# Kernel optimization log

Hardware: AMD Instinct MI355X
Metric: run time of the kernel (lower is better)

Reference implementation:

```python
import jax, jax.numpy as jnp
import numpy as np

N_USERS = 50000
N_ITEMS = 100000
N_GROUPS = 20000
D = 128
NNZ_U = 1000000
NNZ_I = 2000000
NNZ_F = 3000000


def setup_inputs() -> dict:
    key = jax.random.key(0)
    ks = jax.random.split(key, 14)
    user_emb = jax.random.normal(ks[0], (N_USERS, D), jnp.float32)
    item_emb = jax.random.normal(ks[1], (N_ITEMS, D), jnp.float32)
    group_emb = jax.random.normal(ks[2], (N_GROUPS, D), jnp.float32)
    # user hypergraph incidence [N_GROUPS, N_USERS] in COO
    u_rows = jax.random.randint(ks[3], (NNZ_U,), 0, N_GROUPS)
    u_cols = jax.random.randint(ks[4], (NNZ_U,), 0, N_USERS)
    u_vals = jax.random.uniform(ks[5], (NNZ_U,), jnp.float32)
    # item hypergraph incidence [N_GROUPS, N_ITEMS] in COO
    i_rows = jax.random.randint(ks[6], (NNZ_I,), 0, N_GROUPS)
    i_cols = jax.random.randint(ks[7], (NNZ_I,), 0, N_ITEMS)
    i_vals = jax.random.uniform(ks[8], (NNZ_I,), jnp.float32)
    # full hypergraph [N_USERS+N_ITEMS, N_GROUPS] in COO
    f_rows = jax.random.randint(ks[9], (NNZ_F,), 0, N_USERS + N_ITEMS)
    f_cols = jax.random.randint(ks[10], (NNZ_F,), 0, N_GROUPS)
    f_vals = jax.random.uniform(ks[11], (NNZ_F,), jnp.float32)
    # nn.Linear(2D, D): weight [D, 2D], bias [D]
    W_agg = jax.random.normal(ks[12], (D, 2 * D), jnp.float32) * 0.05
    b_agg = jnp.zeros((D,), jnp.float32)
    return dict(user_emb=user_emb, item_emb=item_emb, group_emb=group_emb,
                u_rows=u_rows, u_cols=u_cols, u_vals=u_vals,
                i_rows=i_rows, i_cols=i_cols, i_vals=i_vals,
                f_rows=f_rows, f_cols=f_cols, f_vals=f_vals,
                W_agg=W_agg, b_agg=b_agg)


def _spmm(rows, cols, vals, dense, num_rows):
    # sparse[rows, cols]=vals (COO) @ dense -> [num_rows, d]
    return jax.ops.segment_sum(vals[:, None] * dense[cols], rows, num_segments=num_rows)


def reference(user_emb, item_emb, group_emb,
              u_rows, u_cols, u_vals,
              i_rows, i_cols, i_vals,
              f_rows, f_cols, f_vals,
              W_agg, b_agg):
    user_msg = _spmm(u_rows, u_cols, u_vals, user_emb, N_GROUPS)   # [G, D]
    item_msg = _spmm(i_rows, i_cols, i_vals, item_emb, N_GROUPS)   # [G, D]
    msg = jnp.concatenate([user_msg, item_msg], axis=1) @ W_agg.T + b_agg  # [G, D]
    norm_emb = _spmm(f_rows, f_cols, f_vals, msg, N_USERS + N_ITEMS)       # [U+I, D]
    return (norm_emb, msg)
```

## Files before the change

kernel.cpp:

```cpp
#include <hip/hip_runtime.h>
#include <hip/hip_bf16.h>
#include <stdint.h>

#define N_USERS  50000
#define N_ITEMS  100000
#define N_GROUPS 20000
#define DIM      128
#define TWO_DIM  256
#define N_FULL   (N_USERS + N_ITEMS)

#define NBU  625
#define NBI  1250
#define NBF  2344
#define NBT  (NBU + NBI + NBF)
#define CAP  2048

#define TILE_E 32768
#define NT     184
#define NT_PER_XCD 23

__global__ __launch_bounds__(256) void spmm_atomic(
    const int* __restrict__ rows, const int* __restrict__ cols,
    const float* __restrict__ vals, const float* __restrict__ dense,
    float* __restrict__ out, int nnz)
{
    long long t = (long long)blockIdx.x * blockDim.x + threadIdx.x;
    int e    = (int)(t >> 5);
    int lane = (int)(t & 31);
    if (e >= nnz) return;
    int   r = rows[e];
    int   c = cols[e];
    float v = vals[e];
    float4 x = ((const float4*)(dense + (size_t)c * DIM))[lane];
    float* dst = out + (size_t)r * DIM + lane * 4;
    atomicAdd(dst + 0, v * x.x);
    atomicAdd(dst + 1, v * x.y);
    atomicAdd(dst + 2, v * x.z);
    atomicAdd(dst + 3, v * x.w);
}


__device__ __forceinline__ int bucket_of(long long t,
    const int* __restrict__ u_rows, int nnz_u,
    const int* __restrict__ i_rows, int nnz_i,
    const int* __restrict__ f_rows)
{
    if (t < nnz_u)                          return u_rows[t] >> 5;
    else if (t < (long long)nnz_u + nnz_i)  return NBU + (i_rows[t - nnz_u] >> 4);
    else                                    return NBU + NBI + (f_rows[t - nnz_u - nnz_i] >> 6);
}

__global__ __launch_bounds__(512) void hist_tiles(
    const int* __restrict__ u_rows, int nnz_u,
    const int* __restrict__ i_rows, int nnz_i,
    const int* __restrict__ f_rows, int nnz_f,
    unsigned short* __restrict__ M)
{
    __shared__ int h[NBT];
    int tid = threadIdx.x;
    for (int i = tid; i < NBT; i += 512) h[i] = 0;
    __syncthreads();
    int t = (blockIdx.x & 7) * NT_PER_XCD + (blockIdx.x >> 3);
    long long total = (long long)nnz_u + nnz_i + nnz_f;
    long long base  = (long long)t * TILE_E;
    for (int j = tid; j < TILE_E; j += 512) {
        long long e = base + j;
        if (e >= total) break;
        atomicAdd(&h[bucket_of(e, u_rows, nnz_u, i_rows, nnz_i, f_rows)], 1);
    }
    __syncthreads();
    unsigned short* Mrow = M + (size_t)t * NBT;
    for (int i = tid; i < NBT; i += 512) Mrow[i] = (unsigned short)h[i];
}

__global__ __launch_bounds__(64) void tile_prefix(
    unsigned short* __restrict__ M, int* __restrict__ btot)
{
    int b = blockIdx.x * 64 + threadIdx.x;
    if (b >= NBT) return;
    int run = 0;
#pragma unroll 1
    for (int t = 0; t < NT; t += 4) {
        size_t i0 = (size_t)(t + 0) * NBT + b;
        size_t i1 = (size_t)(t + 1) * NBT + b;
        size_t i2 = (size_t)(t + 2) * NBT + b;
        size_t i3 = (size_t)(t + 3) * NBT + b;
        int v0 = M[i0], v1 = M[i1], v2 = M[i2], v3 = M[i3];
        M[i0] = (unsigned short)run; run += v0;
        M[i1] = (unsigned short)run; run += v1;
        M[i2] = (unsigned short)run; run += v2;
        M[i3] = (unsigned short)run; run += v3;
    }
    btot[b] = run;
}

__global__ __launch_bounds__(256) void scan_buckets(
    const int* __restrict__ btot, int* __restrict__ bptr)
{
    __shared__ int wsum[4];
    __shared__ int s_carry;
    int tid = threadIdx.x, lane = tid & 63, wave = tid >> 6;
    if (tid == 0) s_carry = 0;
    __syncthreads();
    for (int base = 0; base < NBT; base += 256) {
        int b = base + tid;
        int x = (b < NBT) ? btot[b] : 0;
        int incl = x;
#pragma unroll
        for (int off = 1; off < 64; off <<= 1) {
            int y = __shfl_up(incl, off, 64);
            if (lane >= off) incl += y;
        }
        if (lane == 63) wsum[wave] = incl;
        __syncthreads();
        int waveOff = 0;
        for (int w = 0; w < wave; ++w) waveOff += wsum[w];
        int carry = s_carry;
        int ex = carry + waveOff + incl - x;
        if (b < NBT) bptr[b] = ex;
        __syncthreads();
        if (tid == 255) s_carry = carry + waveOff + incl;
        __syncthreads();
    }
    if (tid == 0) bptr[NBT] = s_carry;
}

__global__ __launch_bounds__(512) void scatter_tiles(
    const int* __restrict__ u_rows, const int* __restrict__ u_cols,
    const float* __restrict__ u_vals, int nnz_u,
    const int* __restrict__ i_rows, const int* __restrict__ i_cols,
    const float* __restrict__ i_vals, int nnz_i,
    const int* __restrict__ f_rows, const int* __restrict__ f_cols,
    const float* __restrict__ f_vals, int nnz_f,
    const unsigned short* __restrict__ M, const int* __restrict__ bptr,
    uint2* __restrict__ pack)
{
    __shared__ int cur[NBT];
    int tid = threadIdx.x;
    int t = (blockIdx.x & 7) * NT_PER_XCD + (blockIdx.x >> 3);
    const unsigned short* Mrow = M + (size_t)t * NBT;
    for (int i = tid; i < NBT; i += 512) cur[i] = bptr[i] + (int)Mrow[i];
    __syncthreads();
    long long total = (long long)nnz_u + nnz_i + nnz_f;
    long long base  = (long long)t * TILE_E;
    for (int j = tid; j < TILE_E; j += 512) {
        long long e = base + j;
        if (e >= total) break;
        int b, lrow, col; float v;
        if (e < nnz_u) {
            int k = (int)e; int r = u_rows[k];
            b = r >> 5; lrow = r & 31; col = u_cols[k]; v = u_vals[k];
        } else if (e < (long long)nnz_u + nnz_i) {
            int k = (int)(e - nnz_u); int r = i_rows[k];
            b = NBU + (r >> 4); lrow = r & 15; col = i_cols[k]; v = i_vals[k];
        } else {
            int k = (int)(e - nnz_u - nnz_i); int r = f_rows[k];
            b = NBU + NBI + (r >> 6); lrow = r & 63; col = f_cols[k]; v = f_vals[k];
        }
        int p = atomicAdd(&cur[b], 1);
        pack[p] = make_uint2(((unsigned)lrow << 17) | (unsigned)col, __float_as_uint(v));
    }
}

__global__ __launch_bounds__(256) void gather_buckets(
    const int* __restrict__ bptr, const uint2* __restrict__ pack,
    const float4* __restrict__ denseA, float* __restrict__ outA,
    int nbA, int rowsA, int nrowsA, int baseA,
    const float4* __restrict__ denseB, float* __restrict__ outB,
    int rowsB, int nrowsB, int baseB)
{
    __shared__ uint2 sE[CAP];
    __shared__ int   h[64];
    __shared__ int   o[65];

    const float4* dense; float* out; int rowsPB, nrows, lb, bid;
    if ((int)blockIdx.x < nbA) {
        dense = denseA; out = outA; rowsPB = rowsA; nrows = nrowsA;
        lb = blockIdx.x; bid = baseA + lb;
    } else {
        dense = denseB; out = outB; rowsPB = rowsB; nrows = nrowsB;
        lb = blockIdx.x - nbA; bid = baseB + lb;
    }
    int tid = threadIdx.x;
    if (tid < 64) h[tid] = 0;
    __syncthreads();

    int p0 = bptr[bid], p1 = bptr[bid + 1];
    int cnt = p1 - p0;

    for (int j = tid; j < cnt; j += 256)
        atomicAdd(&h[pack[p0 + j].x >> 17], 1);
    __syncthreads();

    if (tid < 64) {
        int x = (tid < rowsPB) ? h[tid] : 0;
        int incl = x;
#pragma unroll
        for (int off = 1; off < 64; off <<= 1) {
            int y = __shfl_up(incl, off, 64);
            if ((tid & 63) >= off) incl += y;
        }
        o[tid + 1] = incl;
        if (tid == 0) o[0] = 0;
        h[tid] = incl - x;
    }
    __syncthreads();

    for (int j = tid; j < cnt; j += 256) {
        uint2 e = pack[p0 + j];
        int r = e.x >> 17;
        int p = atomicAdd(&h[r], 1);
        sE[p] = make_uint2(e.x & 0x1FFFF, e.y);
    }
    __syncthreads();

    int wave = tid >> 6, lane = tid & 63, half = lane >> 5, sl = lane & 31;
    float4* out4 = (float4*)out;
    for (int r = wave; r < rowsPB; r += 4) {
        int s = o[r], epos = o[r + 1];
        float4 a0 = make_float4(0.f, 0.f, 0.f, 0.f);
        float4 a1 = a0, a2 = a0, a3 = a0;
        for (int base = s; base < epos; base += 8) {
            int j0 = base + half, j1 = base + 2 + half;
            int j2 = base + 4 + half, j3 = base + 6 + half;
            if (j0 < epos) {
                uint2 e = sE[j0]; float v = __uint_as_float(e.y);
                float4 x = dense[(size_t)e.x * 32 + sl];
                a0.x = fmaf(v, x.x, a0.x); a0.y = fmaf(v, x.y, a0.y);
                a0.z = fmaf(v, x.z, a0.z); a0.w = fmaf(v, x.w, a0.w);
            }
            if (j1 < epos) {
                uint2 e = sE[j1]; float v = __uint_as_float(e.y);
                float4 x = dense[(size_t)e.x * 32 + sl];
                a1.x = fmaf(v, x.x, a1.x); a1.y = fmaf(v, x.y, a1.y);
                a1.z = fmaf(v, x.z, a1.z); a1.w = fmaf(v, x.w, a1.w);
            }
            if (j2 < epos) {
                uint2 e = sE[j2]; float v = __uint_as_float(e.y);
                float4 x = dense[(size_t)e.x * 32 + sl];
                a2.x = fmaf(v, x.x, a2.x); a2.y = fmaf(v, x.y, a2.y);
                a2.z = fmaf(v, x.z, a2.z); a2.w = fmaf(v, x.w, a2.w);
            }
            if (j3 < epos) {
                uint2 e = sE[j3]; float v = __uint_as_float(e.y);
                float4 x = dense[(size_t)e.x * 32 + sl];
                a3.x = fmaf(v, x.x, a3.x); a3.y = fmaf(v, x.y, a3.y);
                a3.z = fmaf(v, x.z, a3.z); a3.w = fmaf(v, x.w, a3.w);
            }
        }
        float4 acc;
        acc.x = (a0.x + a1.x) + (a2.x + a3.x);
        acc.y = (a0.y + a1.y) + (a2.y + a3.y);
        acc.z = (a0.z + a1.z) + (a2.z + a3.z);
        acc.w = (a0.w + a1.w) + (a2.w + a3.w);
        acc.x += __shfl_xor(acc.x, 32, 64);
        acc.y += __shfl_xor(acc.y, 32, 64);
        acc.z += __shfl_xor(acc.z, 32, 64);
        acc.w += __shfl_xor(acc.w, 32, 64);
        int row = lb * rowsPB + r;
        if (half == 0 && row < nrows)
            out4[(size_t)row * 32 + sl] = acc;
    }
}

__global__ __launch_bounds__(256) void dense_agg(
    const float* __restrict__ um, const float* __restrict__ im,
    const float* __restrict__ W, const float* __restrict__ b,
    float* __restrict__ msg)
{
    __shared__ float As[32][68];
    __shared__ float Ws[64][132];

    int tid = threadIdx.x;
    int tx  = tid & 15;
    int ty  = tid >> 4;
    int rowBase = blockIdx.x * 32;

    float acc[2][8];
#pragma unroll
    for (int i = 0; i < 2; ++i)
#pragma unroll
        for (int j = 0; j < 8; ++j) acc[i][j] = 0.f;

    for (int kc = 0; kc < 4; ++kc) {
        int k0 = kc * 64;
        const float* Asrc = (k0 < DIM) ? um : im;
        int kOff = (k0 < DIM) ? k0 : (k0 - DIM);

#pragma unroll
        for (int l = 0; l < 2; ++l) {
            int idx = tid + l * 256;
            int r   = idx >> 4;
            int kq  = idx & 15;
            int gRow = rowBase + r;
            float4 v = make_float4(0.f, 0.f, 0.f, 0.f);
            if (gRow < N_GROUPS)
                v = *(const float4*)(Asrc + (size_t)gRow * DIM + kOff + kq * 4);
            *(float4*)&As[r][kq * 4] = v;
        }
#pragma unroll
        for (int l = 0; l < 8; ++l) {
            int idx = tid + l * 256;
            int d   = idx >> 4;
            int kq  = idx & 15;
            float4 v = *(const float4*)(W + (size_t)d * TWO_DIM + k0 + kq * 4);
            Ws[kq * 4 + 0][d] = v.x;
            Ws[kq * 4 + 1][d] = v.y;
            Ws[kq * 4 + 2][d] = v.z;
            Ws[kq * 4 + 3][d] = v.w;
        }
        __syncthreads();

        int ty2 = ty * 2;
        int tx8 = tx * 8;
#pragma unroll 8
        for (int k = 0; k < 64; ++k) {
            float a0 = As[ty2 + 0][k];
            float a1 = As[ty2 + 1][k];
            float4 w0 = *(const float4*)&Ws[k][tx8];
            float4 w1 = *(const float4*)&Ws[k][tx8 + 4];
            acc[0][0] = fmaf(a0, w0.x, acc[0][0]);
            acc[0][1] = fmaf(a0, w0.y, acc[0][1]);
            acc[0][2] = fmaf(a0, w0.z, acc[0][2]);
            acc[0][3] = fmaf(a0, w0.w, acc[0][3]);
            acc[0][4] = fmaf(a0, w1.x, acc[0][4]);
            acc[0][5] = fmaf(a0, w1.y, acc[0][5]);
            acc[0][6] = fmaf(a0, w1.z, acc[0][6]);
            acc[0][7] = fmaf(a0, w1.w, acc[0][7]);
            acc[1][0] = fmaf(a1, w0.x, acc[1][0]);
            acc[1][1] = fmaf(a1, w0.y, acc[1][1]);
            acc[1][2] = fmaf(a1, w0.z, acc[1][2]);
            acc[1][3] = fmaf(a1, w0.w, acc[1][3]);
            acc[1][4] = fmaf(a1, w1.x, acc[1][4]);
            acc[1][5] = fmaf(a1, w1.y, acc[1][5]);
            acc[1][6] = fmaf(a1, w1.z, acc[1][6]);
            acc[1][7] = fmaf(a1, w1.w, acc[1][7]);
        }
        __syncthreads();
    }

    int d0 = tx * 8;
    float4 bv0 = *(const float4*)(b + d0);
    float4 bv1 = *(const float4*)(b + d0 + 4);
#pragma unroll
    for (int i = 0; i < 2; ++i) {
        int gRow = rowBase + ty * 2 + i;
        if (gRow < N_GROUPS) {
            float4 o0 = make_float4(acc[i][0] + bv0.x, acc[i][1] + bv0.y,
                                    acc[i][2] + bv0.z, acc[i][3] + bv0.w);
            float4 o1 = make_float4(acc[i][4] + bv1.x, acc[i][5] + bv1.y,
                                    acc[i][6] + bv1.z, acc[i][7] + bv1.w);
            *(float4*)(msg + (size_t)gRow * DIM + d0)     = o0;
            *(float4*)(msg + (size_t)gRow * DIM + d0 + 4) = o1;
        }
    }
}

extern "C" void kernel_launch(void* const* d_in, const int* in_sizes, int n_in,
                              void* d_out, int out_size, void* d_ws, size_t ws_size,
                              hipStream_t stream)
{
    const float* user_emb = (const float*)d_in[0];
    const float* item_emb = (const float*)d_in[1];
    const int*   u_rows = (const int*)d_in[3];
    const int*   u_cols = (const int*)d_in[4];
    const float* u_vals = (const float*)d_in[5];
    const int*   i_rows = (const int*)d_in[6];
    const int*   i_cols = (const int*)d_in[7];
    const float* i_vals = (const float*)d_in[8];
    const int*   f_rows = (const int*)d_in[9];
    const int*   f_cols = (const int*)d_in[10];
    const float* f_vals = (const float*)d_in[11];
    const float* W      = (const float*)d_in[12];
    const float* bias   = (const float*)d_in[13];

    int nnz_u = in_sizes[3];
    int nnz_i = in_sizes[6];
    int nnz_f = in_sizes[9];
    long long nnz_tot = (long long)nnz_u + nnz_i + nnz_f;

    float* out  = (float*)d_out;
    float* norm = out;
    float* msg  = out + (size_t)N_FULL * DIM;

    float* um = norm;
    float* im = norm + (size_t)N_GROUPS * DIM;

    auto ceil16 = [](size_t b) { return (b + 15) & ~(size_t)15; };
    size_t need = 0;
    size_t o_M    = need; need += ceil16((size_t)NT * NBT * 2);
    size_t o_btot = need; need += ceil16((size_t)NBT * 4);
    size_t o_bptr = need; need += ceil16((size_t)(NBT + 1) * 4);
    size_t o_pack = need; need += ceil16((size_t)nnz_tot * 8);

    if (ws_size >= need && nnz_tot <= (long long)NT * TILE_E) {
        uint8_t* ws = (uint8_t*)d_ws;
        unsigned short* M = (unsigned short*)(ws + o_M);
        int*   btot = (int*)(ws + o_btot);
        int*   bptr = (int*)(ws + o_bptr);
        uint2* pack = (uint2*)(ws + o_pack);

        hist_tiles<<<NT, 512, 0, stream>>>(
            u_rows, nnz_u, i_rows, nnz_i, f_rows, nnz_f, M);

        tile_prefix<<<(NBT + 63) / 64, 64, 0, stream>>>(M, btot);

        scan_buckets<<<1, 256, 0, stream>>>(btot, bptr);

        scatter_tiles<<<NT, 512, 0, stream>>>(
            u_rows, u_cols, u_vals, nnz_u,
            i_rows, i_cols, i_vals, nnz_i,
            f_rows, f_cols, f_vals, nnz_f,
            M, bptr, pack);

        gather_buckets<<<NBU + NBI, 256, 0, stream>>>(
            bptr, pack,
            (const float4*)user_emb, um, NBU, 32, N_GROUPS, 0,
            (const float4*)item_emb, im, 16, N_GROUPS, NBU);

        dense_agg<<<(N_GROUPS + 31) / 32, 256, 0, stream>>>(um, im, W, bias, msg);

        gather_buckets<<<NBF, 256, 0, stream>>>(
            bptr, pack,
            (const float4*)msg, norm, NBF, 64, N_FULL, NBU + NBI,
            (const float4*)msg, norm, 64, N_FULL, NBU + NBI);
    } else {
        hipMemsetAsync(norm, 0, (size_t)N_FULL * DIM * sizeof(float), stream);
        auto spmm_blocks = [](int nnz) {
            return (unsigned)(((long long)nnz * 32 + 255) / 256);
        };
        spmm_atomic<<<spmm_blocks(nnz_u), 256, 0, stream>>>(
            u_rows, u_cols, u_vals, user_emb, um, nnz_u);
        spmm_atomic<<<spmm_blocks(nnz_i), 256, 0, stream>>>(
            i_rows, i_cols, i_vals, item_emb, im, nnz_i);
        dense_agg<<<(N_GROUPS + 31) / 32, 256, 0, stream>>>(um, im, W, bias, msg);
        hipMemsetAsync(norm, 0, (size_t)2 * N_GROUPS * DIM * sizeof(float), stream);
        spmm_atomic<<<spmm_blocks(nnz_f), 256, 0, stream>>>(
            f_rows, f_cols, f_vals, msg, norm, nnz_f);
    }
}
```

Baseline: 821.6 us.

## Gather dense rows from bf16 copies of embeddings and msg in SpMM

Converts user and item embeddings to bf16 in the workspace with a new conversion kernel, and has dense_agg also write a bf16 copy of msg. The gather SpMM kernels then read half-width rows and widen them to fp32 before the FMA, which halves the random-gather traffic. In exchange it adds two conversion passes over the 150k x 128 embedding tables on every call and needs more workspace. It also loses precision on the inputs, which may break tolerance.

```diff
diff --git a/kernel.cpp b/kernel.cpp
--- a/kernel.cpp
+++ b/kernel.cpp
@@ -18,6 +18,26 @@
 #define TILE_E 32768
 #define NT     184
 #define NT_PER_XCD 23
+
+__device__ __forceinline__ unsigned bf16_rne(float f)
+{
+    unsigned u = __float_as_uint(f);
+    return (u + 0x7FFFu + ((u >> 16) & 1u)) >> 16;
+}
+__device__ __forceinline__ unsigned bf16_pack(float a, float b)
+{
+    return bf16_rne(a) | (bf16_rne(b) << 16);
+}
+
+__global__ __launch_bounds__(256) void f32_to_bf16(
+    const float4* __restrict__ src, uint2* __restrict__ dst, int n4)
+{
+    int stride = gridDim.x * 256;
+    for (int i = blockIdx.x * 256 + threadIdx.x; i < n4; i += stride) {
+        float4 v = src[i];
+        dst[i] = make_uint2(bf16_pack(v.x, v.y), bf16_pack(v.z, v.w));
+    }
+}
 
 __global__ __launch_bounds__(256) void spmm_atomic(
     const int* __restrict__ rows, const int* __restrict__ cols,
@@ -38,7 +58,6 @@
     atomicAdd(dst + 2, v * x.z);
     atomicAdd(dst + 3, v * x.w);
 }
-
 
 __device__ __forceinline__ int bucket_of(long long t,
     const int* __restrict__ u_rows, int nnz_u,
@@ -162,18 +181,38 @@
     }
 }
 
+template<bool BF16>
+__device__ __forceinline__ void edge_fma(
+    const void* __restrict__ dense, unsigned col, int sl, float v, float4& a)
+{
+    if constexpr (BF16) {
+        uint2 q = ((const uint2*)dense)[(size_t)col * 32 + sl];
+        float x0 = __uint_as_float(q.x << 16);
+        float x1 = __uint_as_float(q.x & 0xFFFF0000u);
+        float x2 = __uint_as_float(q.y << 16);
+        float x3 = __uint_as_float(q.y & 0xFFFF0000u);
+        a.x = fmaf(v, x0, a.x); a.y = fmaf(v, x1, a.y);
+        a.z = fmaf(v, x2, a.z); a.w = fmaf(v, x3, a.w);
+    } else {
+        float4 x = ((const float4*)dense)[(size_t)col * 32 + sl];
+        a.x = fmaf(v, x.x, a.x); a.y = fmaf(v, x.y, a.y);
+        a.z = fmaf(v, x.z, a.z); a.w = fmaf(v, x.w, a.w);
+    }
+}
+
+template<bool BF16>
 __global__ __launch_bounds__(256) void gather_buckets(
     const int* __restrict__ bptr, const uint2* __restrict__ pack,
-    const float4* __restrict__ denseA, float* __restrict__ outA,
+    const void* __restrict__ denseA, float* __restrict__ outA,
     int nbA, int rowsA, int nrowsA, int baseA,
-    const float4* __restrict__ denseB, float* __restrict__ outB,
+    const void* __restrict__ denseB, float* __restrict__ outB,
     int rowsB, int nrowsB, int baseB)
 {
     __shared__ uint2 sE[CAP];
     __shared__ int   h[64];
     __shared__ int   o[65];
 
-    const float4* dense; float* out; int rowsPB, nrows, lb, bid;
+    const void* dense; float* out; int rowsPB, nrows, lb, bid;
     if ((int)blockIdx.x < nbA) {
         dense = denseA; out = outA; rowsPB = rowsA; nrows = nrowsA;
         lb = blockIdx.x; bid = baseA + lb;
@@ -224,28 +263,20 @@
             int j0 = base + half, j1 = base + 2 + half;
             int j2 = base + 4 + half, j3 = base + 6 + half;
             if (j0 < epos) {
-                uint2 e = sE[j0]; float v = __uint_as_float(e.y);
-                float4 x = dense[(size_t)e.x * 32 + sl];
-                a0.x = fmaf(v, x.x, a0.x); a0.y = fmaf(v, x.y, a0.y);
-                a0.z = fmaf(v, x.z, a0.z); a0.w = fmaf(v, x.w, a0.w);
+                uint2 e = sE[j0];
+                edge_fma<BF16>(dense, e.x, sl, __uint_as_float(e.y), a0);
             }
             if (j1 < epos) {
-                uint2 e = sE[j1]; float v = __uint_as_float(e.y);
-                float4 x = dense[(size_t)e.x * 32 + sl];
-                a1.x = fmaf(v, x.x, a1.x); a1.y = fmaf(v, x.y, a1.y);
-                a1.z = fmaf(v, x.z, a1.z); a1.w = fmaf(v, x.w, a1.w);
+                uint2 e = sE[j1];
+                edge_fma<BF16>(dense, e.x, sl, __uint_as_float(e.y), a1);
             }
             if (j2 < epos) {
-                uint2 e = sE[j2]; float v = __uint_as_float(e.y);
-                float4 x = dense[(size_t)e.x * 32 + sl];
-                a2.x = fmaf(v, x.x, a2.x); a2.y = fmaf(v, x.y, a2.y);
-                a2.z = fmaf(v, x.z, a2.z); a2.w = fmaf(v, x.w, a2.w);
+                uint2 e = sE[j2];
+                edge_fma<BF16>(dense, e.x, sl, __uint_as_float(e.y), a2);
             }
             if (j3 < epos) {
-                uint2 e = sE[j3]; float v = __uint_as_float(e.y);
-                float4 x = dense[(size_t)e.x * 32 + sl];
-                a3.x = fmaf(v, x.x, a3.x); a3.y = fmaf(v, x.y, a3.y);
-                a3.z = fmaf(v, x.z, a3.z); a3.w = fmaf(v, x.w, a3.w);
+                uint2 e = sE[j3];
+                edge_fma<BF16>(dense, e.x, sl, __uint_as_float(e.y), a3);
             }
         }
         float4 acc;
@@ -266,7 +297,7 @@
 __global__ __launch_bounds__(256) void dense_agg(
     const float* __restrict__ um, const float* __restrict__ im,
     const float* __restrict__ W, const float* __restrict__ b,
-    float* __restrict__ msg)
+    float* __restrict__ msg, uint4* __restrict__ msgb)
 {
     __shared__ float As[32][68];
     __shared__ float Ws[64][132];
@@ -352,6 +383,14 @@
                                     acc[i][6] + bv1.z, acc[i][7] + bv1.w);
             *(float4*)(msg + (size_t)gRow * DIM + d0)     = o0;
             *(float4*)(msg + (size_t)gRow * DIM + d0 + 4) = o1;
+            if (msgb) {
+                uint4 pb;
+                pb.x = bf16_pack(o0.x, o0.y);
+                pb.y = bf16_pack(o0.z, o0.w);
+                pb.z = bf16_pack(o1.x, o1.y);
+                pb.w = bf16_pack(o1.z, o1.w);
+                msgb[(size_t)gRow * 16 + tx] = pb;
+            }
         }
     }
 }
@@ -392,13 +431,28 @@
     size_t o_btot = need; need += ceil16((size_t)NBT * 4);
     size_t o_bptr = need; need += ceil16((size_t)(NBT + 1) * 4);
     size_t o_pack = need; need += ceil16((size_t)nnz_tot * 8);
-
-    if (ws_size >= need && nnz_tot <= (long long)NT * TILE_E) {
+    size_t need_base = need;
+    size_t o_ebf  = need; need += ceil16((size_t)(N_USERS + N_ITEMS) * DIM * 2);
+    size_t o_msgb = need; need += ceil16((size_t)N_GROUPS * DIM * 2);
+    size_t need_bf16 = need;
+
+    if (ws_size >= need_base && nnz_tot <= (long long)NT * TILE_E) {
+        bool use_bf16 = (ws_size >= need_bf16);
         uint8_t* ws = (uint8_t*)d_ws;
         unsigned short* M = (unsigned short*)(ws + o_M);
         int*   btot = (int*)(ws + o_btot);
         int*   bptr = (int*)(ws + o_bptr);
         uint2* pack = (uint2*)(ws + o_pack);
+        uint2* ubf  = (uint2*)(ws + o_ebf);
+        uint2* ibf  = ubf + (size_t)N_USERS * 32;
+        uint4* msgb = (uint4*)(ws + o_msgb);
+
+        if (use_bf16) {
+            f32_to_bf16<<<1024, 256, 0, stream>>>(
+                (const float4*)user_emb, ubf, N_USERS * (DIM / 4));
+            f32_to_bf16<<<1024, 256, 0, stream>>>(
+                (const float4*)item_emb, ibf, N_ITEMS * (DIM / 4));
+        }
 
         hist_tiles<<<NT, 512, 0, stream>>>(
             u_rows, nnz_u, i_rows, nnz_i, f_rows, nnz_f, M);
@@ -413,17 +467,33 @@
             f_rows, f_cols, f_vals, nnz_f,
             M, bptr, pack);
 
-        gather_buckets<<<NBU + NBI, 256, 0, stream>>>(
-            bptr, pack,
-            (const float4*)user_emb, um, NBU, 32, N_GROUPS, 0,
-            (const float4*)item_emb, im, 16, N_GROUPS, NBU);
-
-        dense_agg<<<(N_GROUPS + 31) / 32, 256, 0, stream>>>(um, im, W, bias, msg);
-
-        gather_buckets<<<NBF, 256, 0, stream>>>(
-            bptr, pack,
-            (const float4*)msg, norm, NBF, 64, N_FULL, NBU + NBI,
-            (const float4*)msg, norm, 64, N_FULL, NBU + NBI);
+        if (use_bf16) {
+            gather_buckets<true><<<NBU + NBI, 256, 0, stream>>>(
+                bptr, pack,
+                ubf, um, NBU, 32, N_GROUPS, 0,
+                ibf, im, 16, N_GROUPS, NBU);
+
+            dense_agg<<<(N_GROUPS + 31) / 32, 256, 0, stream>>>(
+                um, im, W, bias, msg, msgb);
+
+            gather_buckets<true><<<NBF, 256, 0, stream>>>(
+                bptr, pack,
+                msgb, norm, NBF, 64, N_FULL, NBU + NBI,
+                msgb, norm, 64, N_FULL, NBU + NBI);
+        } else {
+            gather_buckets<false><<<NBU + NBI, 256, 0, stream>>>(
+                bptr, pack,
+                user_emb, um, NBU, 32, N_GROUPS, 0,
+                item_emb, im, 16, N_GROUPS, NBU);
+
+            dense_agg<<<(N_GROUPS + 31) / 32, 256, 0, stream>>>(
+                um, im, W, bias, msg, nullptr);
+
+            gather_buckets<false><<<NBF, 256, 0, stream>>>(
+                bptr, pack,
+                msg, norm, NBF, 64, N_FULL, NBU + NBI,
+                msg, norm, 64, N_FULL, NBU + NBI);
+        }
     } else {
         hipMemsetAsync(norm, 0, (size_t)N_FULL * DIM * sizeof(float), stream);
         auto spmm_blocks = [](int nnz) {
@@ -433,7 +503,8 @@
             u_rows, u_cols, u_vals, user_emb, um, nnz_u);
         spmm_atomic<<<spmm_blocks(nnz_i), 256, 0, stream>>>(
             i_rows, i_cols, i_vals, item_emb, im, nnz_i);
-        dense_agg<<<(N_GROUPS + 31) / 32, 256, 0, stream>>>(um, im, W, bias, msg);
+        dense_agg<<<(N_GROUPS + 31) / 32, 256, 0, stream>>>(
+            um, im, W, bias, msg, nullptr);
         hipMemsetAsync(norm, 0, (size_t)2 * N_GROUPS * DIM * sizeof(float), stream);
         spmm_atomic<<<spmm_blocks(nnz_f), 256, 0, stream>>>(
             f_rows, f_cols, f_vals, msg, norm, nnz_f);
```

Result: faster. 748.0 us (-9.0%).
